# Kernel optimization log

Measured on AMD Instinct MI355X. Metric: run time of the kernel, lower is better.

The kernel has to match this reference:

```python
import jax, jax.numpy as jnp
import numpy as np

WAVE_LEN = 1000.0
DIM_G = 64


def box_relational_embedding(boxes):
    # boxes: (B, N, 4) -> (B, N, N, 64) trigonometric geometry embedding
    B, N, _ = boxes.shape
    x_min, y_min, x_max, y_max = jnp.split(boxes, 4, axis=-1)  # each (B,N,1)
    cx = (x_min + x_max) * 0.5
    cy = (y_min + y_max) * 0.5
    w = (x_max - x_min) + 1.0
    h = (y_max - y_min) + 1.0
    cxT = jnp.swapaxes(cx, 1, 2)  # (B,1,N)
    cyT = jnp.swapaxes(cy, 1, 2)
    dx = jnp.log(jnp.clip(jnp.abs((cx - cxT) / w), 1e-3))  # (B,N,N)
    dy = jnp.log(jnp.clip(jnp.abs((cy - cyT) / h), 1e-3))
    dw = jnp.log(w / jnp.swapaxes(w, 1, 2))
    dh = jnp.log(h / jnp.swapaxes(h, 1, 2))
    pos = jnp.stack([dx, dy, dw, dh], axis=-1)  # (B,N,N,4)
    n_freq = DIM_G // 8  # 8 frequency bands
    dim_mat = 1.0 / (WAVE_LEN ** (jnp.arange(n_freq, dtype=pos.dtype) / n_freq))
    mul = (100.0 * pos)[..., None] * dim_mat  # (B,N,N,4,8)
    mul = mul.reshape(B, N, N, 4 * n_freq)  # (B,N,N,32)
    return jnp.concatenate([jnp.sin(mul), jnp.cos(mul)], axis=-1)  # (B,N,N,64)


def setup_inputs() -> dict:
    key = jax.random.key(0)
    ks = jax.random.split(key, 12)
    B, N, D, H = 32, 196, 1024, 8
    scale = 0.02
    inp = {
        "input_query": jax.random.normal(ks[0], (B, N, D), jnp.float32),
        "input_key": jax.random.normal(ks[1], (B, N, D), jnp.float32),
        "input_value": jax.random.normal(ks[2], (B, N, D), jnp.float32),
        "input_box": jax.random.uniform(ks[3], (B, N, 4), jnp.float32),
        "Wq": jax.random.normal(ks[4], (D, D), jnp.float32) * scale,
        "bq": jnp.zeros((D,), jnp.float32),
        "Wk": jax.random.normal(ks[5], (D, D), jnp.float32) * scale,
        "bk": jnp.zeros((D,), jnp.float32),
        "Wv": jax.random.normal(ks[6], (D, D), jnp.float32) * scale,
        "bv": jnp.zeros((D,), jnp.float32),
        "Wo": jax.random.normal(ks[7], (D, D), jnp.float32) * scale,
        "bo": jnp.zeros((D,), jnp.float32),
        "WG_w": jax.random.normal(ks[8], (H, DIM_G), jnp.float32) * scale,  # 8 stacked (64->1) linears
        "WG_b": jnp.zeros((H,), jnp.float32),
    }
    return inp


def reference(input_query, input_key, input_value, input_box,
              Wq, bq, Wk, bk, Wv, bv, Wo, bo, WG_w, WG_b):
    B, N, D = input_query.shape
    H = WG_w.shape[0]
    dk = D // H
    # relation geometry weights per head: (B,H,N,N)
    geo = box_relational_embedding(input_box)  # (B,N,N,64)
    wg = jax.nn.relu(jnp.einsum('bnmg,hg->bhnm', geo, WG_w) + WG_b[None, :, None, None])
    # projections (torch Linear: x @ W.T + b), reshape to (B,H,N,dk)
    def proj(x, W, b):
        return (x @ W.T + b).reshape(B, N, H, dk).transpose(0, 2, 1, 3)
    q = proj(input_query, Wq, bq)
    k = proj(input_key, Wk, bk)
    v = proj(input_value, Wv, bv)
    scores = jnp.einsum('bhnd,bhmd->bhnm', q, k) / np.sqrt(dk).astype(q.dtype)
    logits = jnp.log(jnp.clip(wg, 1e-6)) + scores
    attn = jax.nn.softmax(logits, axis=-1)  # (B,H,N,N)
    out = jnp.einsum('bhnm,bhmd->bhnd', attn, v)  # (B,H,N,dk)
    out = out.transpose(0, 2, 1, 3).reshape(B, N, D)
    return out @ Wo.T + bo
```

## Files before the change

kernel.cpp:

```cpp
#include <hip/hip_runtime.h>
#include <hip/hip_bf16.h>

typedef __bf16 bf16;
typedef _Float16 half_t;
typedef bf16 bf16x8 __attribute__((ext_vector_type(8)));
typedef bf16 bf16x4 __attribute__((ext_vector_type(4)));
typedef float floatx4 __attribute__((ext_vector_type(4)));

#define B_ 32
#define N_ 196
#define H_ 8
#define D_ 1024
#define DK_ 128
#define BN_ (B_ * N_)
#define BH_ (B_ * H_)
#define NPAD_ 224
#define PSTRIDE_ 232

#define MT_ 49
#define NTILE_ 4
#define KT_ 16

typedef __attribute__((address_space(3))) unsigned int lds_uint;
typedef const __attribute__((address_space(1))) unsigned int glb_uint;

__device__ __forceinline__ void async_copy16(const bf16* g, bf16* l) {
  __builtin_amdgcn_global_load_lds((glb_uint*)g, (lds_uint*)l, 16, 0, 0);
}

__device__ __forceinline__ bf16x8 bzero8() {
  bf16x8 z;
#pragma unroll
  for (int i = 0; i < 8; i++) z[i] = (bf16)0.0f;
  return z;
}

#define BARRIER() asm volatile("s_barrier" ::: "memory")
#define WAITV6() asm volatile("s_waitcnt vmcnt(6)" ::: "memory")
#define WAITV0() asm volatile("s_waitcnt vmcnt(0)" ::: "memory")

__global__ __launch_bounds__(256) void cvt3_kernel(const float* __restrict__ s0,
                                                   const float* __restrict__ s1,
                                                   const float* __restrict__ s2,
                                                   bf16* __restrict__ d0,
                                                   bf16* __restrict__ d1,
                                                   bf16* __restrict__ d2, int n4) {
  const int which = blockIdx.y;
  const float* s = (which == 0) ? s0 : (which == 1) ? s1 : s2;
  bf16* d = (which == 0) ? d0 : (which == 1) ? d1 : d2;
  int i = blockIdx.x * 256 + threadIdx.x;
  if (i >= n4) return;
  float4 v = ((const float4*)s)[i];
  bf16x4 o;
  o[0] = (bf16)v.x;
  o[1] = (bf16)v.y;
  o[2] = (bf16)v.z;
  o[3] = (bf16)v.w;
  *(bf16x4*)(d + (size_t)i * 4) = o;
}

__global__ __launch_bounds__(256) void cvt4_kernel(const float* __restrict__ s0,
                                                   const float* __restrict__ s1,
                                                   const float* __restrict__ s2,
                                                   const float* __restrict__ s3,
                                                   bf16* __restrict__ d0,
                                                   bf16* __restrict__ d1,
                                                   bf16* __restrict__ d2,
                                                   bf16* __restrict__ d3, int n4) {
  const int which = blockIdx.y;
  const float* s = (which == 0) ? s0 : (which == 1) ? s1 : (which == 2) ? s2 : s3;
  bf16* d = (which == 0) ? d0 : (which == 1) ? d1 : (which == 2) ? d2 : d3;
  int i = blockIdx.x * 256 + threadIdx.x;
  if (i >= n4) return;
  float4 v = ((const float4*)s)[i];
  bf16x4 o;
  o[0] = (bf16)v.x;
  o[1] = (bf16)v.y;
  o[2] = (bf16)v.z;
  o[3] = (bf16)v.w;
  *(bf16x4*)(d + (size_t)i * 4) = o;
}

__global__ __launch_bounds__(256) void geo_kernel(const float* __restrict__ box,
                                                  const float* __restrict__ WGw,
                                                  const float* __restrict__ WGb,
                                                  half_t* __restrict__ S) {
  __shared__ float4 wsh[128];
  if (threadIdx.x < 128) wsh[threadIdx.x] = ((const float4*)WGw)[threadIdx.x];
  __syncthreads();

  int tid = blockIdx.x * 256 + threadIdx.x;
  int b = tid / (N_ * N_);
  int rem = tid - b * (N_ * N_);
  int n = rem / N_;
  int m = rem - n * N_;

  float4 bn = ((const float4*)box)[b * N_ + n];
  float4 bm = ((const float4*)box)[b * N_ + m];
  float cxn = (bn.x + bn.z) * 0.5f, cyn = (bn.y + bn.w) * 0.5f;
  float wn = bn.z - bn.x + 1.0f, hn = bn.w - bn.y + 1.0f;
  float cxm = (bm.x + bm.z) * 0.5f, cym = (bm.y + bm.w) * 0.5f;
  float wm = bm.z - bm.x + 1.0f, hm = bm.w - bm.y + 1.0f;

  float pos[4];
  pos[0] = __logf(fmaxf(fabsf((cxn - cxm) / wn), 1e-3f));
  pos[1] = __logf(fmaxf(fabsf((cyn - cym) / hn), 1e-3f));
  pos[2] = __logf(wn / wm);
  pos[3] = __logf(hn / hm);

  const float dims[8] = {1.0f,          0.4216965034f, 0.1778279410f, 0.0749894209f,
                         0.0316227766f, 0.0133352143f, 0.0056234133f, 0.0023713737f};
  float feat[64];
#pragma unroll
  for (int p = 0; p < 4; p++) {
#pragma unroll
    for (int f = 0; f < 8; f++) {
      float a = 100.0f * pos[p] * dims[f];
      feat[p * 8 + f] = __sinf(a);
      feat[32 + p * 8 + f] = __cosf(a);
    }
  }
#pragma unroll
  for (int hh = 0; hh < 8; hh++) {
    float accv = WGb[hh];
#pragma unroll
    for (int g4 = 0; g4 < 16; g4++) {
      float4 wv = wsh[hh * 16 + g4];
      accv += feat[g4 * 4 + 0] * wv.x + feat[g4 * 4 + 1] * wv.y +
              feat[g4 * 4 + 2] * wv.z + feat[g4 * 4 + 3] * wv.w;
    }
    S[((size_t)((b * H_ + hh) * N_ + n)) * NPAD_ + m] = (half_t)fmaxf(accv, 1e-6f);
  }
}

template <int VARIANT>
__global__ __launch_bounds__(512, 1) void gemm8p(
    const bf16* __restrict__ A0, const bf16* __restrict__ A1, const bf16* __restrict__ A2,
    const bf16* __restrict__ W0, const bf16* __restrict__ W1, const bf16* __restrict__ W2,
    const float* __restrict__ b0, const float* __restrict__ b1, const float* __restrict__ b2,
    void* __restrict__ O0, void* __restrict__ O1, void* __restrict__ O2) {
  __shared__ bf16 Asb[3][128 * 64];
  __shared__ bf16 Bsb[3][256 * 64];

  const int z = (VARIANT == 0) ? blockIdx.z : 0;
  const bf16* A = (z == 0) ? A0 : (z == 1) ? A1 : A2;
  const bf16* W = (z == 0) ? W0 : (z == 1) ? W1 : W2;
  const float* bias = (z == 0) ? b0 : (z == 1) ? b1 : b2;

  const int tid = threadIdx.x;
  const int lane = tid & 63;
  const int wid = tid >> 6;
  const int l16 = lane & 15;
  const int quad = lane >> 4;
  const int wm = wid >> 2;
  const int wn = wid & 3;

  const bf16* gA = A + (size_t)blockIdx.y * 128 * D_;
  const bf16* gB = W + (size_t)blockIdx.x * 256 * D_;

  const int srow = tid >> 3;
  const int lslot = (tid & 7) ^ (srow & 7);
  const size_t s0 = (size_t)srow * D_ + lslot * 8;
  const size_t s1 = (size_t)(64 + srow) * D_ + lslot * 8;
  const size_t s2 = (size_t)(128 + srow) * D_ + lslot * 8;
  const size_t s3 = (size_t)(192 + srow) * D_ + lslot * 8;

  int arow[4], brow[4], kslot[2];
#pragma unroll
  for (int i = 0; i < 4; i++) arow[i] = (wm * 64 + i * 16 + l16) * 64;
#pragma unroll
  for (int j = 0; j < 4; j++) brow[j] = (wn * 64 + j * 16 + l16) * 64;
#pragma unroll
  for (int kk = 0; kk < 2; kk++) kslot[kk] = (((kk * 4 + quad) ^ (l16 & 7)) * 8);

  floatx4 acc[4][4];
#pragma unroll
  for (int i = 0; i < 4; i++)
#pragma unroll
    for (int j = 0; j < 4; j++)
#pragma unroll
      for (int r = 0; r < 4; r++) acc[i][j][r] = 0.0f;

#pragma unroll
  for (int kt = 0; kt < 2; kt++) {
    const bf16* sa = gA + kt * 64;
    const bf16* sb = gB + kt * 64;
    async_copy16(sa + s0, &Asb[kt][tid * 8]);
    async_copy16(sa + s1, &Asb[kt][4096 + tid * 8]);
    async_copy16(sb + s0, &Bsb[kt][tid * 8]);
    async_copy16(sb + s1, &Bsb[kt][4096 + tid * 8]);
    async_copy16(sb + s2, &Bsb[kt][8192 + tid * 8]);
    async_copy16(sb + s3, &Bsb[kt][12288 + tid * 8]);
  }
  WAITV6();
  BARRIER();

  for (int kt = 0; kt < KT_; ++kt) {
    const int g = kt % 3;
    const int gn = (kt + 2) % 3;
    const bool pf = (kt + 2 < KT_);
    const bf16* Ab = Asb[g];
    const bf16* Bb = Bsb[g];
    const bf16* pa = gA + (kt + 2) * 64;
    const bf16* pb = gB + (kt + 2) * 64;
    bf16x8 af[2][2], bfv[2][2];
#pragma unroll
    for (int ph = 0; ph < 4; ++ph) {
      const int ih = ph >> 1;
      const int jh = ph & 1;
      if (jh == 0) {
#pragma unroll
        for (int i2 = 0; i2 < 2; i2++)
#pragma unroll
          for (int kk = 0; kk < 2; kk++)
            af[i2][kk] = *(const bf16x8*)(Ab + arow[2 * ih + i2] + kslot[kk]);
      }
#pragma unroll
      for (int j2 = 0; j2 < 2; j2++)
#pragma unroll
        for (int kk = 0; kk < 2; kk++)
          bfv[j2][kk] = *(const bf16x8*)(Bb + brow[2 * jh + j2] + kslot[kk]);
      if (pf) {
        if (ph == 0) {
          async_copy16(pa + s0, &Asb[gn][tid * 8]);
          async_copy16(pa + s1, &Asb[gn][4096 + tid * 8]);
        } else if (ph == 1) {
          async_copy16(pb + s0, &Bsb[gn][tid * 8]);
          async_copy16(pb + s1, &Bsb[gn][4096 + tid * 8]);
        } else if (ph == 2) {
          async_copy16(pb + s2, &Bsb[gn][8192 + tid * 8]);
          async_copy16(pb + s3, &Bsb[gn][12288 + tid * 8]);
        }
      }
      BARRIER();
      __builtin_amdgcn_s_setprio(1);
#pragma unroll
      for (int i2 = 0; i2 < 2; i2++)
#pragma unroll
        for (int j2 = 0; j2 < 2; j2++)
#pragma unroll
          for (int kk = 0; kk < 2; kk++)
            acc[2 * ih + i2][2 * jh + j2] = __builtin_amdgcn_mfma_f32_16x16x32_bf16(
                af[i2][kk], bfv[j2][kk], acc[2 * ih + i2][2 * jh + j2], 0, 0, 0);
      __builtin_amdgcn_s_setprio(0);
      if (ph == 3 && kt < KT_ - 1) {
        if (pf) WAITV6();
        else    WAITV0();
      }
      BARRIER();
    }
  }

  const int m0 = blockIdx.y * 128 + wm * 64;
  const int n0 = blockIdx.x * 256 + wn * 64;
#pragma unroll
  for (int j = 0; j < 4; j++) {
    const int col = n0 + j * 16 + l16;
    const float bv = bias[col];
#pragma unroll
    for (int i = 0; i < 4; i++) {
#pragma unroll
      for (int r = 0; r < 4; r++) {
        const int row = m0 + i * 16 + quad * 4 + r;
        float v = acc[i][j][r] + bv;
        if (VARIANT == 1) {
          ((float*)O0)[(size_t)row * D_ + col] = v;
        } else if (z < 2) {
          bf16* Cout = z ? (bf16*)O1 : (bf16*)O0;
          Cout[(size_t)row * D_ + col] = (bf16)v;
        } else {
          int b = row / N_;
          int n = row - b * N_;
          int h = col >> 7;
          int d = col & (DK_ - 1);
          ((bf16*)O2)[((size_t)((b * H_ + h) * DK_ + d)) * NPAD_ + n] = (bf16)v;
        }
      }
    }
  }
}

__global__ __launch_bounds__(256) void attn_kernel(const bf16* __restrict__ Q,
                                                   const bf16* __restrict__ Kmat,
                                                   const bf16* __restrict__ Vt,
                                                   const half_t* __restrict__ Sb,
                                                   bf16* __restrict__ AO) {
  __shared__ bf16 Pl[4 * 16 * PSTRIDE_];

  const int f = blockIdx.x;
  const int tile = (f >> 3) & 3;
  const int bh = (f & 7) | ((f >> 5) << 3);
  const int b = bh >> 3;
  const int h = bh & 7;
  const int wave = threadIdx.x >> 6;
  const int lane = threadIdx.x & 63;
  const int l16 = lane & 15;
  const int quad = lane >> 4;
  const int nrb = tile * 64 + wave * 16;

  floatx4 S[14];
#pragma unroll
  for (int j = 0; j < 14; j++)
#pragma unroll
    for (int r = 0; r < 4; r++) S[j][r] = 0.0f;

  const int na = nrb + l16;
  const bool nav = na < N_;
  const bf16* aptr = Q + ((size_t)(b * N_ + (nav ? na : 0))) * D_ + h * DK_ + quad * 8;
  bf16x8 afr[4];
#pragma unroll
  for (int kk = 0; kk < 4; kk++) afr[kk] = nav ? *(const bf16x8*)(aptr + kk * 32) : bzero8();

#pragma unroll
  for (int j = 0; j < 14; j++) {
    const int m = j * 16 + l16;
    const bool mv = m < N_;
    const bf16* kp = Kmat + ((size_t)(b * N_ + (mv ? m : 0))) * D_ + h * DK_ + quad * 8;
#pragma unroll
    for (int kk = 0; kk < 4; kk++) {
      bf16x8 bb = mv ? *(const bf16x8*)(kp + kk * 32) : bzero8();
      S[j] = __builtin_amdgcn_mfma_f32_16x16x32_bf16(afr[kk], bb, S[j], 0, 0, 0);
    }
  }

  const float scale = 0.08838834764831845f;
  const half_t* bbase = Sb + ((size_t)bh * N_) * NPAD_;
  bf16* pw = Pl + wave * 16 * PSTRIDE_;
  float inv[4];
#pragma unroll
  for (int r = 0; r < 4; r++) {
    const int n = nrb + quad * 4 + r;
    const size_t brow = (size_t)(n < N_ ? n : 0) * NPAD_;
    float mx = S[0][r] * scale;
#pragma unroll
    for (int j = 0; j < 14; j++) {
      S[j][r] *= scale;
      mx = fmaxf(mx, S[j][r]);
    }
#pragma unroll
    for (int off = 1; off < 16; off <<= 1) mx = fmaxf(mx, __shfl_xor(mx, off, 64));
    float sum = 0.0f;
#pragma unroll
    for (int j = 0; j < 14; j++) {
      const int m = j * 16 + l16;
      float w = (m < N_) ? (float)bbase[brow + m] : 0.0f;
      float e = w * __expf(S[j][r] - mx);
      sum += e;
      pw[(quad * 4 + r) * PSTRIDE_ + m] = (bf16)e;
    }
#pragma unroll
    for (int off = 1; off < 16; off <<= 1) sum += __shfl_xor(sum, off, 64);
    inv[r] = 1.0f / sum;
  }
  __syncthreads();

  floatx4 O[8];
#pragma unroll
  for (int j2 = 0; j2 < 8; j2++)
#pragma unroll
    for (int r = 0; r < 4; r++) O[j2][r] = 0.0f;

  const bf16* vbase = Vt + (size_t)bh * DK_ * NPAD_ + quad * 8;
  const bf16* pr = pw + l16 * PSTRIDE_ + quad * 8;
#pragma unroll
  for (int k0 = 0; k0 < NPAD_; k0 += 32) {
    bf16x8 a = *(const bf16x8*)(pr + k0);
#pragma unroll
    for (int j2 = 0; j2 < 8; j2++) {
      bf16x8 bb = *(const bf16x8*)(vbase + (size_t)(j2 * 16 + l16) * NPAD_ + k0);
      O[j2] = __builtin_amdgcn_mfma_f32_16x16x32_bf16(a, bb, O[j2], 0, 0, 0);
    }
  }

#pragma unroll
  for (int r = 0; r < 4; r++) {
    const int n = nrb + quad * 4 + r;
    if (n < N_) {
#pragma unroll
      for (int j2 = 0; j2 < 8; j2++) {
        AO[((size_t)(b * N_ + n)) * D_ + h * DK_ + j2 * 16 + l16] = (bf16)(O[j2][r] * inv[r]);
      }
    }
  }
}

extern "C" void kernel_launch(void* const* d_in, const int* in_sizes, int n_in,
                              void* d_out, int out_size, void* d_ws, size_t ws_size,
                              hipStream_t stream) {
  const float* xq = (const float*)d_in[0];
  const float* xk = (const float*)d_in[1];
  const float* xv = (const float*)d_in[2];
  const float* box = (const float*)d_in[3];
  const float* Wq = (const float*)d_in[4];
  const float* bq = (const float*)d_in[5];
  const float* Wk = (const float*)d_in[6];
  const float* bk = (const float*)d_in[7];
  const float* Wv = (const float*)d_in[8];
  const float* bv = (const float*)d_in[9];
  const float* Wo = (const float*)d_in[10];
  const float* bo = (const float*)d_in[11];
  const float* WGw = (const float*)d_in[12];
  const float* WGb = (const float*)d_in[13];

  size_t off = 0;
  char* wsc = (char*)d_ws;
  auto alloc = [&](size_t bytes) -> void* {
    void* p = wsc + off;
    off += (bytes + 255) & ~(size_t)255;
    return p;
  };
  bf16* xq_b = (bf16*)alloc((size_t)BN_ * D_ * 2);
  bf16* xk_b = (bf16*)alloc((size_t)BN_ * D_ * 2);
  bf16* xv_b = (bf16*)alloc((size_t)BN_ * D_ * 2);
  bf16* wq_b = (bf16*)alloc((size_t)D_ * D_ * 2);
  bf16* wk_b = (bf16*)alloc((size_t)D_ * D_ * 2);
  bf16* wv_b = (bf16*)alloc((size_t)D_ * D_ * 2);
  bf16* wo_b = (bf16*)alloc((size_t)D_ * D_ * 2);
  bf16* q_b = (bf16*)alloc((size_t)BN_ * D_ * 2);
  bf16* k_b = (bf16*)alloc((size_t)BN_ * D_ * 2);
  bf16* vt_b = (bf16*)alloc((size_t)BH_ * DK_ * NPAD_ * 2);
  bf16* ao_b = (bf16*)alloc((size_t)BN_ * D_ * 2);
  half_t* S = (half_t*)alloc((size_t)BH_ * N_ * NPAD_ * 2);

  const int n4x = BN_ * D_ / 4;
  const int n4w = D_ * D_ / 4;
  dim3 g3(n4x / 256, 3, 1);
  cvt3_kernel<<<g3, 256, 0, stream>>>(xq, xk, xv, xq_b, xk_b, xv_b, n4x);
  dim3 g4(n4w / 256, 4, 1);
  cvt4_kernel<<<g4, 256, 0, stream>>>(Wq, Wk, Wv, Wo, wq_b, wk_b, wv_b, wo_b, n4w);

  geo_kernel<<<(B_ * N_ * N_) / 256, 256, 0, stream>>>(box, WGw, WGb, S);

  hipMemsetAsync(vt_b, 0, (size_t)BH_ * DK_ * NPAD_ * 2, stream);

  dim3 gqkv(NTILE_, MT_, 3);
  gemm8p<0><<<gqkv, 512, 0, stream>>>(xq_b, xk_b, xv_b, wq_b, wk_b, wv_b, bq, bk, bv,
                                      q_b, k_b, vt_b);

  attn_kernel<<<1024, 256, 0, stream>>>(q_b, k_b, vt_b, S, ao_b);

  dim3 gout(NTILE_, MT_, 1);
  gemm8p<1><<<gout, 512, 0, stream>>>(ao_b, nullptr, nullptr, wo_b, nullptr, nullptr,
                                      bo, nullptr, nullptr, d_out, nullptr, nullptr);
}
```

Measured before the change: 370.2 us.

## Replace 512-thread triple-buffered GEMM with 256-thread double-buffered 128x128 tiles

Rewrites the projection GEMMs to use 128x128 output tiles with 4 waves, 2 blocks per CU, and two LDS stages instead of three, with one barrier per K step. The goal is higher occupancy and less barrier overhead, at the cost of halving B-tile reuse and giving up the deeper prefetch. It also wraps the MFMA calls in the attention kernel with s_setprio raises.

Measured after the change: 355.7 us. 1.04x faster.

```diff
diff --git a/kernel.cpp b/kernel.cpp
--- a/kernel.cpp
+++ b/kernel.cpp
@@ -17,8 +17,6 @@
 #define NPAD_ 224
 #define PSTRIDE_ 232
 
-#define MT_ 49
-#define NTILE_ 4
 #define KT_ 16
 
 typedef __attribute__((address_space(3))) unsigned int lds_uint;
@@ -36,7 +34,6 @@
 }
 
 #define BARRIER() asm volatile("s_barrier" ::: "memory")
-#define WAITV6() asm volatile("s_waitcnt vmcnt(6)" ::: "memory")
 #define WAITV0() asm volatile("s_waitcnt vmcnt(0)" ::: "memory")
 
 __global__ __launch_bounds__(256) void cvt3_kernel(const float* __restrict__ s0,
@@ -134,13 +131,13 @@
 }
 
 template <int VARIANT>
-__global__ __launch_bounds__(512, 1) void gemm8p(
+__global__ __launch_bounds__(256, 2) void gemm2p(
     const bf16* __restrict__ A0, const bf16* __restrict__ A1, const bf16* __restrict__ A2,
     const bf16* __restrict__ W0, const bf16* __restrict__ W1, const bf16* __restrict__ W2,
     const float* __restrict__ b0, const float* __restrict__ b1, const float* __restrict__ b2,
     void* __restrict__ O0, void* __restrict__ O1, void* __restrict__ O2) {
-  __shared__ bf16 Asb[3][128 * 64];
-  __shared__ bf16 Bsb[3][256 * 64];
+  __shared__ bf16 As[2][128 * 64];
+  __shared__ bf16 Bs[2][128 * 64];
 
   const int z = (VARIANT == 0) ? blockIdx.z : 0;
   const bf16* A = (z == 0) ? A0 : (z == 1) ? A1 : A2;
@@ -152,18 +149,17 @@
   const int wid = tid >> 6;
   const int l16 = lane & 15;
   const int quad = lane >> 4;
-  const int wm = wid >> 2;
-  const int wn = wid & 3;
+  const int wm = wid >> 1;
+  const int wn = wid & 1;
 
   const bf16* gA = A + (size_t)blockIdx.y * 128 * D_;
-  const bf16* gB = W + (size_t)blockIdx.x * 256 * D_;
+  const bf16* gB = W + (size_t)blockIdx.x * 128 * D_;
 
   const int srow = tid >> 3;
   const int lslot = (tid & 7) ^ (srow & 7);
-  const size_t s0 = (size_t)srow * D_ + lslot * 8;
-  const size_t s1 = (size_t)(64 + srow) * D_ + lslot * 8;
-  const size_t s2 = (size_t)(128 + srow) * D_ + lslot * 8;
-  const size_t s3 = (size_t)(192 + srow) * D_ + lslot * 8;
+  size_t sOff[4];
+#pragma unroll
+  for (int u = 0; u < 4; u++) sOff[u] = (size_t)(u * 32 + srow) * D_ + lslot * 8;
 
   int arow[4], brow[4], kslot[2];
 #pragma unroll
@@ -171,7 +167,7 @@
 #pragma unroll
   for (int j = 0; j < 4; j++) brow[j] = (wn * 64 + j * 16 + l16) * 64;
 #pragma unroll
-  for (int kk = 0; kk < 2; kk++) kslot[kk] = (((kk * 4 + quad) ^ (l16 & 7)) * 8);
+  for (int kk = 0; kk < 2; kk++) kslot[kk] = ((kk * 4 + quad) ^ (l16 & 7)) * 8;
 
   floatx4 acc[4][4];
 #pragma unroll
@@ -182,77 +178,64 @@
       for (int r = 0; r < 4; r++) acc[i][j][r] = 0.0f;
 
 #pragma unroll
-  for (int kt = 0; kt < 2; kt++) {
-    const bf16* sa = gA + kt * 64;
-    const bf16* sb = gB + kt * 64;
-    async_copy16(sa + s0, &Asb[kt][tid * 8]);
-    async_copy16(sa + s1, &Asb[kt][4096 + tid * 8]);
-    async_copy16(sb + s0, &Bsb[kt][tid * 8]);
-    async_copy16(sb + s1, &Bsb[kt][4096 + tid * 8]);
-    async_copy16(sb + s2, &Bsb[kt][8192 + tid * 8]);
-    async_copy16(sb + s3, &Bsb[kt][12288 + tid * 8]);
-  }
-  WAITV6();
+  for (int u = 0; u < 4; u++) {
+    async_copy16(gA + sOff[u], &As[0][u * 2048 + tid * 8]);
+    async_copy16(gB + sOff[u], &Bs[0][u * 2048 + tid * 8]);
+  }
+  WAITV0();
   BARRIER();
 
   for (int kt = 0; kt < KT_; ++kt) {
-    const int g = kt % 3;
-    const int gn = (kt + 2) % 3;
-    const bool pf = (kt + 2 < KT_);
-    const bf16* Ab = Asb[g];
-    const bf16* Bb = Bsb[g];
-    const bf16* pa = gA + (kt + 2) * 64;
-    const bf16* pb = gB + (kt + 2) * 64;
-    bf16x8 af[2][2], bfv[2][2];
-#pragma unroll
-    for (int ph = 0; ph < 4; ++ph) {
-      const int ih = ph >> 1;
-      const int jh = ph & 1;
-      if (jh == 0) {
-#pragma unroll
-        for (int i2 = 0; i2 < 2; i2++)
-#pragma unroll
-          for (int kk = 0; kk < 2; kk++)
-            af[i2][kk] = *(const bf16x8*)(Ab + arow[2 * ih + i2] + kslot[kk]);
-      }
-#pragma unroll
-      for (int j2 = 0; j2 < 2; j2++)
-#pragma unroll
-        for (int kk = 0; kk < 2; kk++)
-          bfv[j2][kk] = *(const bf16x8*)(Bb + brow[2 * jh + j2] + kslot[kk]);
-      if (pf) {
-        if (ph == 0) {
-          async_copy16(pa + s0, &Asb[gn][tid * 8]);
-          async_copy16(pa + s1, &Asb[gn][4096 + tid * 8]);
-        } else if (ph == 1) {
-          async_copy16(pb + s0, &Bsb[gn][tid * 8]);
-          async_copy16(pb + s1, &Bsb[gn][4096 + tid * 8]);
-        } else if (ph == 2) {
-          async_copy16(pb + s2, &Bsb[gn][8192 + tid * 8]);
-          async_copy16(pb + s3, &Bsb[gn][12288 + tid * 8]);
-        }
-      }
+    const int cur = kt & 1;
+    const bf16* Ab = As[cur];
+    const bf16* Bb = Bs[cur];
+    const bool pf = (kt + 1 < KT_);
+    const bf16* pa = gA + (kt + 1) * 64;
+    const bf16* pb = gB + (kt + 1) * 64;
+    bf16* dA = As[cur ^ 1];
+    bf16* dB = Bs[cur ^ 1];
+    bf16x8 af[4], bfv[4];
+
+#pragma unroll
+    for (int i = 0; i < 4; i++) af[i] = *(const bf16x8*)(Ab + arow[i] + kslot[0]);
+#pragma unroll
+    for (int j = 0; j < 4; j++) bfv[j] = *(const bf16x8*)(Bb + brow[j] + kslot[0]);
+    if (pf) {
+#pragma unroll
+      for (int u = 0; u < 4; u++) async_copy16(pa + sOff[u], dA + u * 2048 + tid * 8);
+    }
+    __builtin_amdgcn_s_setprio(1);
+#pragma unroll
+    for (int i = 0; i < 4; i++)
+#pragma unroll
+      for (int j = 0; j < 4; j++)
+        acc[i][j] = __builtin_amdgcn_mfma_f32_16x16x32_bf16(af[i], bfv[j], acc[i][j], 0, 0, 0);
+    __builtin_amdgcn_s_setprio(0);
+
+#pragma unroll
+    for (int i = 0; i < 4; i++) af[i] = *(const bf16x8*)(Ab + arow[i] + kslot[1]);
+#pragma unroll
+    for (int j = 0; j < 4; j++) bfv[j] = *(const bf16x8*)(Bb + brow[j] + kslot[1]);
+    if (pf) {
+#pragma unroll
+      for (int u = 0; u < 4; u++) async_copy16(pb + sOff[u], dB + u * 2048 + tid * 8);
+    }
+    __builtin_amdgcn_s_setprio(1);
+#pragma unroll
+    for (int i = 0; i < 4; i++)
+#pragma unroll
+      for (int j = 0; j < 4; j++)
+        acc[i][j] = __builtin_amdgcn_mfma_f32_16x16x32_bf16(af[i], bfv[j], acc[i][j], 0, 0, 0);
+    __builtin_amdgcn_s_setprio(0);
+
+    if (pf) {
+      WAITV0();
       BARRIER();
-      __builtin_amdgcn_s_setprio(1);
-#pragma unroll
-      for (int i2 = 0; i2 < 2; i2++)
-#pragma unroll
-        for (int j2 = 0; j2 < 2; j2++)
-#pragma unroll
-          for (int kk = 0; kk < 2; kk++)
-            acc[2 * ih + i2][2 * jh + j2] = __builtin_amdgcn_mfma_f32_16x16x32_bf16(
-                af[i2][kk], bfv[j2][kk], acc[2 * ih + i2][2 * jh + j2], 0, 0, 0);
-      __builtin_amdgcn_s_setprio(0);
-      if (ph == 3 && kt < KT_ - 1) {
-        if (pf) WAITV6();
-        else    WAITV0();
-      }
-      BARRIER();
     }
   }
 
   const int m0 = blockIdx.y * 128 + wm * 64;
-  const int n0 = blockIdx.x * 256 + wn * 64;
+  const int n0 = blockIdx.x * 128 + wn * 64;
 #pragma unroll
   for (int j = 0; j < 4; j++) {
     const int col = n0 + j * 16 + l16;
@@ -319,7 +302,9 @@
 #pragma unroll
     for (int kk = 0; kk < 4; kk++) {
       bf16x8 bb = mv ? *(const bf16x8*)(kp + kk * 32) : bzero8();
+      __builtin_amdgcn_s_setprio(1);
       S[j] = __builtin_amdgcn_mfma_f32_16x16x32_bf16(afr[kk], bb, S[j], 0, 0, 0);
+      __builtin_amdgcn_s_setprio(0);
     }
   }
 
@@ -368,7 +353,9 @@
 #pragma unroll
     for (int j2 = 0; j2 < 8; j2++) {
       bf16x8 bb = *(const bf16x8*)(vbase + (size_t)(j2 * 16 + l16) * NPAD_ + k0);
+      __builtin_amdgcn_s_setprio(1);
       O[j2] = __builtin_amdgcn_mfma_f32_16x16x32_bf16(a, bb, O[j2], 0, 0, 0);
+      __builtin_amdgcn_s_setprio(0);
     }
   }
 
@@ -433,13 +420,13 @@
 
   hipMemsetAsync(vt_b, 0, (size_t)BH_ * DK_ * NPAD_ * 2, stream);
 
-  dim3 gqkv(NTILE_, MT_, 3);
-  gemm8p<0><<<gqkv, 512, 0, stream>>>(xq_b, xk_b, xv_b, wq_b, wk_b, wv_b, bq, bk, bv,
+  dim3 gqkv(D_ / 128, BN_ / 128, 3);
+  gemm2p<0><<<gqkv, 256, 0, stream>>>(xq_b, xk_b, xv_b, wq_b, wk_b, wv_b, bq, bk, bv,
                                       q_b, k_b, vt_b);
 
   attn_kernel<<<1024, 256, 0, stream>>>(q_b, k_b, vt_b, S, ao_b);
 
-  dim3 gout(NTILE_, MT_, 1);
-  gemm8p<1><<<gout, 512, 0, stream>>>(ao_b, nullptr, nullptr, wo_b, nullptr, nullptr,
+  dim3 gout(D_ / 128, BN_ / 128, 1);
+  gemm2p<1><<<gout, 256, 0, stream>>>(ao_b, nullptr, nullptr, wo_b, nullptr, nullptr,
                                       bo, nullptr, nullptr, d_out, nullptr, nullptr);
 }
```
